# Kernel optimization log

Hardware: AMD Instinct MI355X
Metric: run time of the kernel (lower is better)

The kernel has to match this reference:

```python
import jax, jax.numpy as jnp
import numpy as np

B, K, V = 128, 8, 50257   # batch, beam_size, num_syms
L, MAXL = 64, 128         # current cand seq length, max_seq_len
A, D = 512, 1024          # attention_dim, decoder_dim
EOS = 2
NEG = -1.0e9


def setup_inputs() -> dict:
    key = jax.random.key(0)
    ks = jax.random.split(key, 9)
    return {
        "logits": jax.random.normal(ks[0], (B, K, V), dtype=jnp.float32),
        "cand_scores": jax.random.normal(ks[1], (B, K), dtype=jnp.float32),
        "cand_seqs": jax.random.randint(ks[2], (B, K, L), 0, V, dtype=jnp.int32),
        "completed_scores": jax.random.normal(ks[3], (B, K), dtype=jnp.float32),
        "completed_seqs": jax.random.randint(ks[4], (B, K, MAXL), 0, V, dtype=jnp.int32),
        "completed_length": jax.random.randint(ks[5], (B, K), 1, MAXL, dtype=jnp.int32),
        "decoder_context": jax.random.normal(ks[6], (B * K, A), dtype=jnp.float32),
        "decoder_rnn1": jax.random.normal(ks[7], (B * K, D), dtype=jnp.float32),
        "decoder_rnn2": jax.random.normal(ks[8], (B * K, D), dtype=jnp.float32),
    }


def reference(logits, cand_scores, cand_seqs, completed_scores, completed_seqs,
              completed_length, decoder_context, decoder_rnn1, decoder_rnn2):
    # --- beam_search_score: normalize logits, accumulate path scores ---
    logprobs = jax.nn.log_softmax(logits, axis=2)            # [B,K,V]
    new_scores = logprobs + cand_scores[:, :, None]          # [B,K,V]

    # --- deal_with_completed: append eos-terminated hyps, length-normalized top-k ---
    eos_scores = new_scores[:, :, EOS]                                   # [B,K]
    comp_scores = jnp.concatenate([completed_scores, eos_scores], 1)     # [B,2K]
    eos_tail = jnp.full((B, K, MAXL - L), EOS, dtype=cand_seqs.dtype)
    new_comp_seqs = jnp.concatenate([cand_seqs, eos_tail], 2)            # [B,K,MAXL]
    comp_seqs = jnp.concatenate([completed_seqs, new_comp_seqs], 1)      # [B,2K,MAXL]
    comp_len = jnp.concatenate(
        [completed_length, jnp.full((B, K), L + 1, dtype=completed_length.dtype)], 1)
    rescaled = comp_scores / comp_len.astype(comp_scores.dtype)
    _, cinds = jax.lax.top_k(rescaled, K)                                # [B,K]
    comp_scores = jnp.take_along_axis(comp_scores, cinds, axis=1)
    comp_seqs = jnp.take_along_axis(comp_seqs, cinds[:, :, None], axis=1)
    comp_len = jnp.take_along_axis(comp_len, cinds, axis=1)

    # --- deal_with_uncompleted: top-k over beam*vocab excluding eos ---
    masked = new_scores.at[:, :, EOS].set(NEG)
    flat = masked.reshape(B, K * V)
    new_cand_scores, inds = jax.lax.top_k(flat, K)                       # [B,K]
    parents = inds // V                                                  # [B,K]
    syms = (inds % V).astype(cand_seqs.dtype)
    new_seqs = jnp.take_along_axis(cand_seqs, parents[:, :, None], axis=1)
    new_seqs = jnp.concatenate([new_seqs, syms[:, :, None]], axis=2)     # [B,K,L+1]

    # reorder decoder states by parent beam index
    pidx = parents[:, :, None]
    ctx = jnp.take_along_axis(decoder_context.reshape(B, K, A), pidx, axis=1).reshape(-1, A)
    r1 = jnp.take_along_axis(decoder_rnn1.reshape(B, K, D), pidx, axis=1).reshape(-1, D)
    r2 = jnp.take_along_axis(decoder_rnn2.reshape(B, K, D), pidx, axis=1).reshape(-1, D)

    return (new_cand_scores, new_seqs, parents, comp_scores, comp_seqs, comp_len, ctx, r1, r2)
```

## Files before the change

kernel.cpp:

```cpp
#include <hip/hip_runtime.h>


#define BB 128
#define KK 8
#define VV 50257
#define LL 64
#define MAXLEN 128
#define AA 512
#define DD 1024
#define EOSI 2
#define NTHR 256
#define CAP 2048

constexpr size_t O0 = 0;
constexpr size_t O1 = 1024;
constexpr size_t O2 = 67584;
constexpr size_t O3 = 68608;
constexpr size_t O4 = 69632;
constexpr size_t O5 = 200704;
constexpr size_t O6 = 201728;
constexpr size_t O7 = 726016;
constexpr size_t O8 = 1774592;

__device__ __forceinline__ bool better(float v2, int i2, float v1, int i1) {
  return (v2 > v1) || (v2 == v1 && i2 < i1);
}

__global__ __launch_bounds__(NTHR) void k_rowpass(
    const float* __restrict__ logits,
    float* __restrict__ ws_max, float* __restrict__ ws_lse,
    float* __restrict__ ws_eos,
    float* __restrict__ ws_tv, int* __restrict__ ws_ti) {
  const int r = blockIdx.x;
  const int tid = threadIdx.x;
  const int lane = tid & 63, wid = tid >> 6;
  const float* __restrict__ row = logits + (size_t)r * VV;

  __shared__ float sm[NTHR];
  __shared__ float red[8];
  __shared__ float stau;
  __shared__ int scnt;
  __shared__ float cv[CAP];
  __shared__ int ci[CAP];
  __shared__ float rv4[4]; __shared__ int ri4[4], rl4[4];

  if (tid == 0) { ws_eos[r] = row[EOSI]; scnt = 0; }

  const int pre = (4 - (r & 3)) & 3;
  const int nvec = (VV - pre) >> 2;
  const int rem = VV - pre - (nvec << 2);
  const float4* __restrict__ vrow = (const float4*)(row + pre);

  float m = -INFINITY, s0 = 0.0f, s1 = 0.0f;
  if (tid < pre) { float x = row[tid]; s0 += __expf(x); m = fmaxf(m, x); }
  if (tid >= 8 && tid < 8 + rem) {
    float x = row[pre + (nvec << 2) + (tid - 8)];
    s0 += __expf(x); m = fmaxf(m, x);
  }
  for (int i = tid; i < nvec; i += NTHR) {
    float4 x = vrow[i];
    s0 += __expf(x.x); s1 += __expf(x.y);
    s0 += __expf(x.z); s1 += __expf(x.w);
    m = fmaxf(fmaxf(x.x, x.y), m);
    m = fmaxf(fmaxf(x.z, x.w), m);
  }
  float s = s0 + s1;
  sm[tid] = m;
  float mr = m;
  for (int off = 32; off; off >>= 1) {
    s += __shfl_down(s, off);
    mr = fmaxf(mr, __shfl_down(mr, off));
  }
  if (lane == 0) { red[wid] = s; red[4 + wid] = mr; }
  __syncthreads();
  if (tid == 0) {
    float S = (red[0] + red[1]) + (red[2] + red[3]);
    float M = fmaxf(fmaxf(red[4], red[5]), fmaxf(red[6], red[7]));
    ws_max[r] = M;
    ws_lse[r] = logf(S) - M;
  }

  if (wid == 0) {
    float v0 = sm[lane], v1 = sm[lane + 64], v2 = sm[lane + 128], v3 = sm[lane + 192];
    float tau = -INFINITY;
    for (int rr = 0; rr < 9; ++rr) {
      float lm = fmaxf(fmaxf(v0, v1), fmaxf(v2, v3));
      float wm = lm;
      for (int off = 32; off; off >>= 1) wm = fmaxf(wm, __shfl_down(wm, off));
      wm = __shfl(wm, 0);
      tau = wm;
      unsigned long long msk = __ballot(lm == wm);
      int first = __ffsll((unsigned long long)msk) - 1;
      if (lane == first) {
        if (v0 == wm) v0 = -INFINITY;
        else if (v1 == wm) v1 = -INFINITY;
        else if (v2 == wm) v2 = -INFINITY;
        else v3 = -INFINITY;
      }
    }
    if (lane == 0) stau = tau;
  }
  __syncthreads();
  const float tau = stau;

  if (tid < pre) {
    float x = row[tid];
    if (x >= tau) { int p = atomicAdd(&scnt, 1); if (p < CAP) { cv[p] = x; ci[p] = tid; } }
  }
  if (tid >= 8 && tid < 8 + rem) {
    int e = pre + (nvec << 2) + (tid - 8);
    float x = row[e];
    if (x >= tau) { int p = atomicAdd(&scnt, 1); if (p < CAP) { cv[p] = x; ci[p] = e; } }
  }
  for (int i = tid; i < nvec; i += NTHR) {
    float4 x = vrow[i];
    if (x.x >= tau || x.y >= tau || x.z >= tau || x.w >= tau) {
      int i0 = pre + (i << 2);
      if (x.x >= tau) { int p = atomicAdd(&scnt, 1); if (p < CAP) { cv[p] = x.x; ci[p] = i0; } }
      if (x.y >= tau) { int p = atomicAdd(&scnt, 1); if (p < CAP) { cv[p] = x.y; ci[p] = i0 + 1; } }
      if (x.z >= tau) { int p = atomicAdd(&scnt, 1); if (p < CAP) { cv[p] = x.z; ci[p] = i0 + 2; } }
      if (x.w >= tau) { int p = atomicAdd(&scnt, 1); if (p < CAP) { cv[p] = x.w; ci[p] = i0 + 3; } }
    }
  }
  __syncthreads();

  int n = scnt < CAP ? scnt : CAP;
  for (int sel = 0; sel < 8; ++sel) {
    float bv = -INFINITY; int bi = 0x7fffffff; int bl = -1;
    for (int j = tid; j < n; j += NTHR) {
      float v = cv[j]; int idx = ci[j];
      if (idx != EOSI && better(v, idx, bv, bi)) { bv = v; bi = idx; bl = j; }
    }
    for (int off = 32; off; off >>= 1) {
      float v2 = __shfl_down(bv, off);
      int i2 = __shfl_down(bi, off);
      int l2 = __shfl_down(bl, off);
      if (better(v2, i2, bv, bi)) { bv = v2; bi = i2; bl = l2; }
    }
    if (lane == 0) { rv4[wid] = bv; ri4[wid] = bi; rl4[wid] = bl; }
    __syncthreads();
    if (tid == 0) {
      float fv = rv4[0]; int fi = ri4[0], fl = rl4[0];
      for (int w = 1; w < 4; ++w)
        if (better(rv4[w], ri4[w], fv, fi)) { fv = rv4[w]; fi = ri4[w]; fl = rl4[w]; }
      ws_tv[r * 8 + sel] = fv;
      ws_ti[r * 8 + sel] = fi;
      if (fl >= 0) cv[fl] = -INFINITY;
    }
    __syncthreads();
  }
}

__global__ __launch_bounds__(NTHR) void k_select(
    const float* __restrict__ cand_scores, const int* __restrict__ cand_seqs,
    const float* __restrict__ completed_scores, const int* __restrict__ completed_seqs,
    const int* __restrict__ completed_length,
    const float* __restrict__ ws_max, const float* __restrict__ ws_lse,
    const float* __restrict__ ws_eos, const float* __restrict__ ws_tv,
    const int* __restrict__ ws_ti, int* __restrict__ ws_par,
    float* __restrict__ out) {
  const int b = blockIdx.x;
  const int tid = threadIdx.x;
  __shared__ float sh_mx[KK], sh_lse[KK], sh_cand[KK];
  __shared__ float sh_ncs[KK]; __shared__ int sh_par[KK], sh_sym[KK];
  __shared__ float sh_cs[KK];  __shared__ int sh_clen[KK], sh_cind[KK];
  if (tid < KK) {
    sh_mx[tid] = ws_max[b * KK + tid];
    sh_lse[tid] = ws_lse[b * KK + tid];
    sh_cand[tid] = cand_scores[b * KK + tid];
  }
  __syncthreads();
  if (tid < 64) {
    const int lane = tid;
    const int k = lane >> 3, j = lane & 7;
    float x = ws_tv[(b * KK + k) * 8 + j];
    int v = ws_ti[(b * KK + k) * 8 + j];
    float val = ((x - sh_mx[k]) - sh_lse[k]) + sh_cand[k];
    int flat = k * VV + v;
    if (v == 0x7fffffff) { val = -INFINITY; flat = 0x7fffffff; }
    for (int sel = 0; sel < 8; ++sel) {
      float bv = val; int bi = flat; int bl = lane;
      for (int off = 32; off; off >>= 1) {
        float v2 = __shfl_down(bv, off);
        int i2 = __shfl_down(bi, off);
        int l2 = __shfl_down(bl, off);
        if (better(v2, i2, bv, bi)) { bv = v2; bi = i2; bl = l2; }
      }
      int wl = __shfl(bl, 0);
      if (lane == wl) {
        sh_ncs[sel] = val; sh_par[sel] = flat / VV; sh_sym[sel] = flat % VV;
        val = -INFINITY; flat = 0x7fffffff;
      }
    }
    float cs; int clen;
    if (lane < KK) {
      cs = completed_scores[b * KK + lane];
      clen = completed_length[b * KK + lane];
    } else if (lane < 2 * KK) {
      int k2 = lane - KK;
      cs = ((ws_eos[b * KK + k2] - sh_mx[k2]) - sh_lse[k2]) + sh_cand[k2];
      clen = LL + 1;
    } else { cs = -INFINITY; clen = 1; }
    float rsc = (lane < 2 * KK) ? cs / (float)clen : -INFINITY;
    for (int sel = 0; sel < 8; ++sel) {
      float bv = rsc; int bi = lane;
      for (int off = 32; off; off >>= 1) {
        float v2 = __shfl_down(bv, off);
        int i2 = __shfl_down(bi, off);
        if (better(v2, i2, bv, bi)) { bv = v2; bi = i2; }
      }
      int wl = __shfl(bi, 0);
      if (lane == wl) {
        sh_cs[sel] = cs; sh_clen[sel] = clen; sh_cind[sel] = lane;
        rsc = -INFINITY;
      }
    }
  }
  __syncthreads();
  if (tid < KK) {
    out[O0 + (size_t)b * KK + tid] = sh_ncs[tid];
    out[O2 + (size_t)b * KK + tid] = (float)sh_par[tid];
    out[O3 + (size_t)b * KK + tid] = sh_cs[tid];
    out[O5 + (size_t)b * KK + tid] = (float)sh_clen[tid];
    ws_par[b * KK + tid] = sh_par[tid];
  }
  for (int t = tid; t < KK * (LL + 1); t += NTHR) {
    int i = t / (LL + 1), pos = t - i * (LL + 1);
    int val;
    if (pos < LL) val = cand_seqs[((size_t)b * KK + sh_par[i]) * LL + pos];
    else val = sh_sym[i];
    out[O1 + ((size_t)b * KK + i) * (LL + 1) + pos] = (float)val;
  }
  for (int t = tid; t < KK * MAXLEN; t += NTHR) {
    int i = t >> 7, pos = t & 127;
    int c = sh_cind[i];
    int val;
    if (c < KK) val = completed_seqs[((size_t)b * KK + c) * MAXLEN + pos];
    else {
      int k2 = c - KK;
      val = (pos < LL) ? cand_seqs[((size_t)b * KK + k2) * LL + pos] : EOSI;
    }
    out[O4 + ((size_t)b * KK + i) * MAXLEN + pos] = (float)val;
  }
}

__global__ __launch_bounds__(NTHR) void k_gather(
    const float* __restrict__ ctx, const float* __restrict__ r1,
    const float* __restrict__ r2, const int* __restrict__ ws_par,
    float* __restrict__ out) {
  const int r = blockIdx.x;
  const int b = r >> 3;
  const int src = (b << 3) + ws_par[r];
  const int tid = threadIdx.x;
  {
    const float4* s4 = (const float4*)(ctx + (size_t)src * AA);
    float4* d4 = (float4*)(out + O6 + (size_t)r * AA);
    for (int i = tid; i < AA / 4; i += NTHR) d4[i] = s4[i];
  }
  {
    const float4* s4 = (const float4*)(r1 + (size_t)src * DD);
    float4* d4 = (float4*)(out + O7 + (size_t)r * DD);
    for (int i = tid; i < DD / 4; i += NTHR) d4[i] = s4[i];
  }
  {
    const float4* s4 = (const float4*)(r2 + (size_t)src * DD);
    float4* d4 = (float4*)(out + O8 + (size_t)r * DD);
    for (int i = tid; i < DD / 4; i += NTHR) d4[i] = s4[i];
  }
}

extern "C" void kernel_launch(void* const* d_in, const int* in_sizes, int n_in,
                              void* d_out, int out_size, void* d_ws, size_t ws_size,
                              hipStream_t stream) {
  const float* logits = (const float*)d_in[0];
  const float* cand_scores = (const float*)d_in[1];
  const int* cand_seqs = (const int*)d_in[2];
  const float* completed_scores = (const float*)d_in[3];
  const int* completed_seqs = (const int*)d_in[4];
  const int* completed_length = (const int*)d_in[5];
  const float* dctx = (const float*)d_in[6];
  const float* drnn1 = (const float*)d_in[7];
  const float* drnn2 = (const float*)d_in[8];
  float* out = (float*)d_out;

  float* ws_max = (float*)d_ws;
  float* ws_lse = ws_max + BB * KK;
  float* ws_eos = ws_lse + BB * KK;
  float* ws_tv = ws_eos + BB * KK;
  int* ws_ti = (int*)(ws_tv + BB * KK * 8);
  int* ws_par = ws_ti + BB * KK * 8;

  k_rowpass<<<BB * KK, NTHR, 0, stream>>>(logits, ws_max, ws_lse, ws_eos, ws_tv, ws_ti);
  k_select<<<BB, NTHR, 0, stream>>>(cand_scores, cand_seqs, completed_scores,
                                    completed_seqs, completed_length, ws_max, ws_lse,
                                    ws_eos, ws_tv, ws_ti, ws_par, out);
  k_gather<<<BB * KK, NTHR, 0, stream>>>(dctx, drnn1, drnn2, ws_par, out);
}
```

Measured before the change: 357.4 us.

## Use 1024-thread row pass with per-segment maxima to skip rescanning the row

The row pass now runs 1024 threads per row and records a maximum for each 64-vector segment, giving 256 segments. The top-9 threshold is taken from these segment maxima, and the candidate-collection pass re-reads only the segments whose maximum reaches the threshold instead of rescanning the whole row. This removes most of the second read of each logits row, at the cost of larger blocks and an extra shuffle reduction per iteration. The boundary elements are now always pushed into the candidate buffer, and the buffer capacity drops to 1024.

Result: slower. 405.5 us (+13.5%).

```diff
diff --git a/kernel.cpp b/kernel.cpp
--- a/kernel.cpp
+++ b/kernel.cpp
@@ -9,8 +9,11 @@
 #define AA 512
 #define DD 1024
 #define EOSI 2
-#define NTHR 256
-#define CAP 2048
+#define NTHR 1024
+#define NWAVE 16
+#define NSEG 256
+#define CAP 1024
+#define STHR 256
 
 constexpr size_t O0 = 0;
 constexpr size_t O1 = 1024;
@@ -36,52 +39,71 @@
   const int lane = tid & 63, wid = tid >> 6;
   const float* __restrict__ row = logits + (size_t)r * VV;
 
-  __shared__ float sm[NTHR];
-  __shared__ float red[8];
+  __shared__ float segmax[NSEG];
+  __shared__ float redS[NWAVE], redM[NWAVE];
   __shared__ float stau;
-  __shared__ int scnt;
+  __shared__ int scnt, snq;
   __shared__ float cv[CAP];
   __shared__ int ci[CAP];
-  __shared__ float rv4[4]; __shared__ int ri4[4], rl4[4];
-
-  if (tid == 0) { ws_eos[r] = row[EOSI]; scnt = 0; }
+  __shared__ int qseg[NSEG];
+  __shared__ float rv4[NWAVE]; __shared__ int ri4[NWAVE], rl4[NWAVE];
+
+  if (tid < NSEG) segmax[tid] = -INFINITY;
+  if (tid == 0) { ws_eos[r] = row[EOSI]; scnt = 0; snq = 0; }
+  __syncthreads();
 
   const int pre = (4 - (r & 3)) & 3;
   const int nvec = (VV - pre) >> 2;
   const int rem = VV - pre - (nvec << 2);
   const float4* __restrict__ vrow = (const float4*)(row + pre);
+  const int niter = (nvec + NTHR - 1) / NTHR;
 
   float m = -INFINITY, s0 = 0.0f, s1 = 0.0f;
-  if (tid < pre) { float x = row[tid]; s0 += __expf(x); m = fmaxf(m, x); }
+
+  if (tid < pre) {
+    float x = row[tid];
+    s0 += __expf(x); m = fmaxf(m, x);
+    int p = atomicAdd(&scnt, 1); cv[p] = x; ci[p] = tid;
+  }
   if (tid >= 8 && tid < 8 + rem) {
-    float x = row[pre + (nvec << 2) + (tid - 8)];
+    int e = pre + (nvec << 2) + (tid - 8);
+    float x = row[e];
     s0 += __expf(x); m = fmaxf(m, x);
-  }
-  for (int i = tid; i < nvec; i += NTHR) {
-    float4 x = vrow[i];
-    s0 += __expf(x.x); s1 += __expf(x.y);
-    s0 += __expf(x.z); s1 += __expf(x.w);
-    m = fmaxf(fmaxf(x.x, x.y), m);
-    m = fmaxf(fmaxf(x.z, x.w), m);
-  }
+    int p = atomicAdd(&scnt, 1); cv[p] = x; ci[p] = e;
+  }
+
+  for (int i = 0; i < niter; ++i) {
+    const int vi = i * NTHR + tid;
+    float mloc = -INFINITY;
+    if (vi < nvec) {
+      float4 x = vrow[vi];
+      s0 += __expf(x.x); s1 += __expf(x.y);
+      s0 += __expf(x.z); s1 += __expf(x.w);
+      mloc = fmaxf(fmaxf(x.x, x.y), fmaxf(x.z, x.w));
+      m = fmaxf(m, mloc);
+    }
+    float wm = mloc;
+    for (int off = 32; off; off >>= 1) wm = fmaxf(wm, __shfl_down(wm, off));
+    if (lane == 0) segmax[i * NWAVE + wid] = wm;
+  }
+
   float s = s0 + s1;
-  sm[tid] = m;
-  float mr = m;
   for (int off = 32; off; off >>= 1) {
     s += __shfl_down(s, off);
-    mr = fmaxf(mr, __shfl_down(mr, off));
-  }
-  if (lane == 0) { red[wid] = s; red[4 + wid] = mr; }
+    m = fmaxf(m, __shfl_down(m, off));
+  }
+  if (lane == 0) { redS[wid] = s; redM[wid] = m; }
   __syncthreads();
   if (tid == 0) {
-    float S = (red[0] + red[1]) + (red[2] + red[3]);
-    float M = fmaxf(fmaxf(red[4], red[5]), fmaxf(red[6], red[7]));
+    float S = 0.0f, M = -INFINITY;
+    for (int w = 0; w < NWAVE; ++w) { S += redS[w]; M = fmaxf(M, redM[w]); }
     ws_max[r] = M;
     ws_lse[r] = logf(S) - M;
   }
 
   if (wid == 0) {
-    float v0 = sm[lane], v1 = sm[lane + 64], v2 = sm[lane + 128], v3 = sm[lane + 192];
+    float v0 = segmax[lane], v1 = segmax[lane + 64];
+    float v2 = segmax[lane + 128], v3 = segmax[lane + 192];
     float tau = -INFINITY;
     for (int rr = 0; rr < 9; ++rr) {
       float lm = fmaxf(fmaxf(v0, v1), fmaxf(v2, v3));
@@ -90,7 +112,7 @@
       wm = __shfl(wm, 0);
       tau = wm;
       unsigned long long msk = __ballot(lm == wm);
-      int first = __ffsll((unsigned long long)msk) - 1;
+      int first = __ffsll(msk) - 1;
       if (lane == first) {
         if (v0 == wm) v0 = -INFINITY;
         else if (v1 == wm) v1 = -INFINITY;
@@ -103,19 +125,18 @@
   __syncthreads();
   const float tau = stau;
 
-  if (tid < pre) {
-    float x = row[tid];
-    if (x >= tau) { int p = atomicAdd(&scnt, 1); if (p < CAP) { cv[p] = x; ci[p] = tid; } }
-  }
-  if (tid >= 8 && tid < 8 + rem) {
-    int e = pre + (nvec << 2) + (tid - 8);
-    float x = row[e];
-    if (x >= tau) { int p = atomicAdd(&scnt, 1); if (p < CAP) { cv[p] = x; ci[p] = e; } }
-  }
-  for (int i = tid; i < nvec; i += NTHR) {
-    float4 x = vrow[i];
-    if (x.x >= tau || x.y >= tau || x.z >= tau || x.w >= tau) {
-      int i0 = pre + (i << 2);
+  if (tid < NSEG && segmax[tid] >= tau) {
+    int p = atomicAdd(&snq, 1);
+    qseg[p] = tid;
+  }
+  __syncthreads();
+  const int nq = snq;
+
+  for (int j = wid; j < nq; j += NWAVE) {
+    const int vi = qseg[j] * 64 + lane;
+    if (vi < nvec) {
+      float4 x = vrow[vi];
+      const int i0 = pre + (vi << 2);
       if (x.x >= tau) { int p = atomicAdd(&scnt, 1); if (p < CAP) { cv[p] = x.x; ci[p] = i0; } }
       if (x.y >= tau) { int p = atomicAdd(&scnt, 1); if (p < CAP) { cv[p] = x.y; ci[p] = i0 + 1; } }
       if (x.z >= tau) { int p = atomicAdd(&scnt, 1); if (p < CAP) { cv[p] = x.z; ci[p] = i0 + 2; } }
@@ -124,7 +145,7 @@
   }
   __syncthreads();
 
-  int n = scnt < CAP ? scnt : CAP;
+  const int n = scnt < CAP ? scnt : CAP;
   for (int sel = 0; sel < 8; ++sel) {
     float bv = -INFINITY; int bi = 0x7fffffff; int bl = -1;
     for (int j = tid; j < n; j += NTHR) {
@@ -141,7 +162,7 @@
     __syncthreads();
     if (tid == 0) {
       float fv = rv4[0]; int fi = ri4[0], fl = rl4[0];
-      for (int w = 1; w < 4; ++w)
+      for (int w = 1; w < NWAVE; ++w)
         if (better(rv4[w], ri4[w], fv, fi)) { fv = rv4[w]; fi = ri4[w]; fl = rl4[w]; }
       ws_tv[r * 8 + sel] = fv;
       ws_ti[r * 8 + sel] = fi;
@@ -151,7 +172,7 @@
   }
 }
 
-__global__ __launch_bounds__(NTHR) void k_select(
+__global__ __launch_bounds__(STHR) void k_select(
     const float* __restrict__ cand_scores, const int* __restrict__ cand_seqs,
     const float* __restrict__ completed_scores, const int* __restrict__ completed_seqs,
     const int* __restrict__ completed_length,
@@ -224,14 +245,14 @@
     out[O5 + (size_t)b * KK + tid] = (float)sh_clen[tid];
     ws_par[b * KK + tid] = sh_par[tid];
   }
-  for (int t = tid; t < KK * (LL + 1); t += NTHR) {
+  for (int t = tid; t < KK * (LL + 1); t += STHR) {
     int i = t / (LL + 1), pos = t - i * (LL + 1);
     int val;
     if (pos < LL) val = cand_seqs[((size_t)b * KK + sh_par[i]) * LL + pos];
     else val = sh_sym[i];
     out[O1 + ((size_t)b * KK + i) * (LL + 1) + pos] = (float)val;
   }
-  for (int t = tid; t < KK * MAXLEN; t += NTHR) {
+  for (int t = tid; t < KK * MAXLEN; t += STHR) {
     int i = t >> 7, pos = t & 127;
     int c = sh_cind[i];
     int val;
@@ -244,7 +265,7 @@
   }
 }
 
-__global__ __launch_bounds__(NTHR) void k_gather(
+__global__ __launch_bounds__(STHR) void k_gather(
     const float* __restrict__ ctx, const float* __restrict__ r1,
     const float* __restrict__ r2, const int* __restrict__ ws_par,
     float* __restrict__ out) {
@@ -255,17 +276,17 @@
   {
     const float4* s4 = (const float4*)(ctx + (size_t)src * AA);
     float4* d4 = (float4*)(out + O6 + (size_t)r * AA);
-    for (int i = tid; i < AA / 4; i += NTHR) d4[i] = s4[i];
+    for (int i = tid; i < AA / 4; i += STHR) d4[i] = s4[i];
   }
   {
     const float4* s4 = (const float4*)(r1 + (size_t)src * DD);
     float4* d4 = (float4*)(out + O7 + (size_t)r * DD);
-    for (int i = tid; i < DD / 4; i += NTHR) d4[i] = s4[i];
+    for (int i = tid; i < DD / 4; i += STHR) d4[i] = s4[i];
   }
   {
     const float4* s4 = (const float4*)(r2 + (size_t)src * DD);
     float4* d4 = (float4*)(out + O8 + (size_t)r * DD);
-    for (int i = tid; i < DD / 4; i += NTHR) d4[i] = s4[i];
+    for (int i = tid; i < DD / 4; i += STHR) d4[i] = s4[i];
   }
 }
 
@@ -291,8 +312,8 @@
   int* ws_par = ws_ti + BB * KK * 8;
 
   k_rowpass<<<BB * KK, NTHR, 0, stream>>>(logits, ws_max, ws_lse, ws_eos, ws_tv, ws_ti);
-  k_select<<<BB, NTHR, 0, stream>>>(cand_scores, cand_seqs, completed_scores,
+  k_select<<<BB, STHR, 0, stream>>>(cand_scores, cand_seqs, completed_scores,
                                     completed_seqs, completed_length, ws_max, ws_lse,
                                     ws_eos, ws_tv, ws_ti, ws_par, out);
-  k_gather<<<BB * KK, NTHR, 0, stream>>>(dctx, drnn1, drnn2, ws_par, out);
-}
+  k_gather<<<BB * KK, STHR, 0, stream>>>(dctx, drnn1, drnn2, ws_par, out);
+}
```
